# Performance work log

Hardware: AMD Instinct MI355X
Metric: run time of the kernel (lower is better)

The kernel has to match this reference:

```python
import jax, jax.numpy as jnp
import numpy as np

EPSILON = float(np.finfo(np.float32).tiny)
K = 32                 # self.k
TRAIN_ENSEMBLE = 2     # repeat_sample in train mode
TAU = 0.1


def setup_inputs() -> dict:
    key = jax.random.key(0)
    scores = jax.random.normal(key, (256, 8192, 4), dtype=jnp.float32)  # [bsz, Nmax, ensemble]
    return {"scores": scores}


def reference(scores):
    bsz, Nmax, ensemble = scores.shape
    repeat = TRAIN_ENSEMBLE
    local_k = min(K, Nmax)

    # flat_scores: (bsz*ensemble, Nmax), then repeated over samples -> (repeat*bsz*ensemble, Nmax)
    flat = scores.transpose(0, 2, 1).reshape(bsz * ensemble, Nmax)
    flat = jnp.tile(flat, (repeat, 1))

    # Gumbel(0,1) noise (m.sample())
    g = jax.random.gumbel(jax.random.key(42), flat.shape, dtype=flat.dtype)
    flat = flat + g

    zeros = jnp.zeros_like(flat)

    def step(carry, _):
        f, khot, onehot = carry
        khot_mask = jnp.maximum(1.0 - onehot, EPSILON)
        f = f + jnp.log(khot_mask)
        onehot = jax.nn.softmax(f / TAU, axis=1)
        return (f, khot + onehot, onehot), None

    (_, khot, _), _ = jax.lax.scan(step, (flat, zeros, zeros), None, length=local_k)

    # hard top-k straight-through
    _, ind = jax.lax.top_k(khot, local_k)                      # (R, local_k)
    rows = jnp.arange(khot.shape[0])[:, None]
    khot_hard = jnp.zeros_like(khot).at[rows, ind].set(1.0)
    res = khot_hard - jax.lax.stop_gradient(khot) + khot

    # (repeat, bsz, ensemble, Nmax) -> (repeat, bsz, Nmax, ensemble)
    new_mask = res.reshape(repeat, bsz, ensemble, Nmax).transpose(0, 1, 3, 2)
    return new_mask
```

## Files before the change

### kernel.cpp

```cpp
#include <hip/hip_runtime.h>

#define TPB 256
#define ROWN 8192
#define CMAX 1024
#define EPS_TINY 1.1754943508222875e-38f

__device__ __forceinline__ unsigned rotl32(unsigned x, int r) {
  return (x << r) | (x >> (32 - r));
}

__device__ __forceinline__ unsigned tf_pxor(unsigned idx) {
  const unsigned ks0 = 0u, ks1 = 42u, ks2 = 0x1BD11BDAu ^ 0u ^ 42u;
  unsigned x0 = ks0;
  unsigned x1 = idx + ks1;
#define TF4(a,b,cc,d) \
  x0 += x1; x1 = rotl32(x1,(a));  x1 ^= x0; \
  x0 += x1; x1 = rotl32(x1,(b));  x1 ^= x0; \
  x0 += x1; x1 = rotl32(x1,(cc)); x1 ^= x0; \
  x0 += x1; x1 = rotl32(x1,(d));  x1 ^= x0;
  TF4(13,15,26,6)   x0 += ks1; x1 += ks2 + 1u;
  TF4(17,29,16,24)  x0 += ks2; x1 += ks0 + 2u;
  TF4(13,15,26,6)   x0 += ks0; x1 += ks1 + 3u;
  TF4(17,29,16,24)  x0 += ks1; x1 += ks2 + 4u;
  TF4(13,15,26,6)   x0 += ks2; x1 += ks0 + 5u;
#undef TF4
  return x0 ^ x1;
}

__device__ __forceinline__ float gumbel_of(unsigned idx) {
  const unsigned bits = tf_pxor(idx);
  float u = __uint_as_float((bits >> 9) | 0x3f800000u) - 1.0f;
  u = u + EPS_TINY;
  u = fmaxf(EPS_TINY, u);
  return -logf(-logf(u));
}

__device__ __forceinline__ float approx_gumbel(unsigned bits) {
  float u = __uint_as_float((bits >> 9) | 0x3f800000u) - 1.0f;
  u = u + EPS_TINY;
  u = fmaxf(EPS_TINY, u);
  float t;
  if (u >= 0.75f) {
    const float v = 1.0f - u;
    t = v * (1.0f + v * (0.5f + v * (0.33333334f + v * (0.25f + v * 0.2f))));
  } else {
    t = -0.69314718f * __log2f(u);
  }
  return -0.69314718f * __log2f(t);
}

__device__ __forceinline__ unsigned key16_of(float x) {
  const unsigned b = __float_as_uint(x) >> 16;
  return (b & 0x8000u) ? (0xFFFFu & ~b) : (b | 0x8000u);
}

__global__ __launch_bounds__(TPB, 8)
void topk_row(const void* __restrict__ scores_raw,
              float* __restrict__ khotArr,
              unsigned short* __restrict__ idxArr,
              int* __restrict__ cntArr) {
  const int t    = threadIdx.x;
  const int lane = t & 63;
  const int wave = t >> 6;

  const int i   = blockIdx.x;
  const int xcd = i & 7;
  const int k   = i >> 3;
  const int e   = k & 3;
  const int q   = k >> 2;
  const int b   = xcd * 32 + (q & 31);
  const int rep = q >> 5;
  const int r   = rep * 1024 + b * 4 + e;
  const unsigned gbase = (unsigned)r * (unsigned)ROWN;

  __shared__ unsigned       kLds[16][TPB];
  __shared__ unsigned short candIdx[CMAX];
  __shared__ float redM[2][4];
  __shared__ float redZ[2][4];
  __shared__ int   wtot[13][4];
  __shared__ int   f32flag;

  if (t == 0) f32flag = 0;
  __syncthreads();
  {
    const unsigned* w = (const unsigned*)scores_raw;
    bool bad = false;
#pragma unroll
    for (int p = 0; p < 4; ++p) {
      const unsigned x = w[t + 256 * p];
      const float flo = __uint_as_float((x & 0xFFFFu) << 16);
      const float fhi = __uint_as_float(x & 0xFFFF0000u);
      if (!(fabsf(flo) <= 16.0f) || !(fabsf(fhi) <= 16.0f)) bad = true;
    }
    if (bad) f32flag = 1;
  }
  __syncthreads();
  const bool in_f32 = (f32flag != 0);

  const size_t ebase0 = ((size_t)b * ROWN + (size_t)t) * 4 + (size_t)e;
  float m = -3.4e38f;
  {
    unsigned pair = 0u;
    if (in_f32) {
      const float* sp = (const float*)scores_raw;
#pragma unroll
      for (int j = 0; j < 32; ++j) {
        const float fj = sp[ebase0 + (size_t)(256 * j) * 4]
                       + approx_gumbel(tf_pxor(gbase + (unsigned)(t + 256 * j)));
        m = fmaxf(m, fj);
        const unsigned kk = key16_of(fj);
        if (j & 1) { pair |= kk << 16; kLds[j >> 1][t] = pair; }
        else pair = kk;
      }
    } else {
      const unsigned short* sp = (const unsigned short*)scores_raw;
#pragma unroll
      for (int j = 0; j < 32; ++j) {
        const float fj = __uint_as_float(((unsigned)sp[ebase0 + (size_t)(256 * j) * 4]) << 16)
                       + approx_gumbel(tf_pxor(gbase + (unsigned)(t + 256 * j)));
        m = fmaxf(m, fj);
        const unsigned kk = key16_of(fj);
        if (j & 1) { pair |= kk << 16; kLds[j >> 1][t] = pair; }
        else pair = kk;
      }
    }
  }

#pragma unroll
  for (int off = 32; off >= 1; off >>= 1) m = fmaxf(m, __shfl_xor(m, off));
  if (lane == 0) redM[0][wave] = m;
  __syncthreads();
  m = fmaxf(fmaxf(redM[0][0], redM[0][1]), fmaxf(redM[0][2], redM[0][3]));

  float lo = m - 25.0f, hi = m;
#pragma unroll 1
  for (int itb = 0; itb < 7; ++itb) {
    const float mid = 0.5f * (lo + hi);
    const unsigned kmid = key16_of(mid);
    int c = 0;
#pragma unroll
    for (int h = 0; h < 16; ++h) {
      const unsigned w = kLds[h][t];
      c += ((w & 0xFFFFu) > kmid) ? 1 : 0;
      c += ((w >> 16) > kmid) ? 1 : 0;
    }
#pragma unroll
    for (int off = 32; off >= 1; off >>= 1) c += __shfl_xor(c, off);
    if (lane == 0) wtot[itb][wave] = c;
    __syncthreads();
    const int tot = wtot[itb][0] + wtot[itb][1] + wtot[itb][2] + wtot[itb][3];
    if (tot >= 33) lo = mid; else hi = mid;
  }
  const float theta = lo - 2.34f;
  const unsigned ktheta = key16_of(theta);

  int cj = 0;
#pragma unroll
  for (int h = 0; h < 16; ++h) {
    const unsigned w = kLds[h][t];
    cj += ((w & 0xFFFFu) >= ktheta) ? 1 : 0;
    cj += ((w >> 16) >= ktheta) ? 1 : 0;
  }
  int incv = cj;
#pragma unroll
  for (int off = 1; off < 64; off <<= 1) {
    const int v = __shfl_up(incv, off);
    if (lane >= off) incv += v;
  }
  if (lane == 63) wtot[12][wave] = incv;
  __syncthreads();
  int base = 0;
  for (int w = 0; w < wave; ++w) base += wtot[12][w];
  int cnt = wtot[12][0] + wtot[12][1] + wtot[12][2] + wtot[12][3];
  if (cnt > CMAX) cnt = CMAX;
  int o = base + incv - cj;
#pragma unroll
  for (int h = 0; h < 16; ++h) {
    const unsigned w = kLds[h][t];
    if ((w & 0xFFFFu) >= ktheta) {
      if (o < CMAX) candIdx[o] = (unsigned short)(t + 256 * (2 * h));
      ++o;
    }
    if ((w >> 16) >= ktheta) {
      if (o < CMAX) candIdx[o] = (unsigned short)(t + 256 * (2 * h + 1));
      ++o;
    }
  }
  __syncthreads();

  float cfr[4], khr[4];
#pragma unroll
  for (int p = 0; p < 4; ++p) {
    cfr[p] = -3.0e38f; khr[p] = -3.0e38f;
    if (256 * p < cnt) {
      const int ci = t + 256 * p;
      if (ci < cnt) {
        const int n = (int)candIdx[ci];
        const size_t ei = ((size_t)b * ROWN + (size_t)n) * 4 + (size_t)e;
        float sc;
        if (in_f32) sc = ((const float*)scores_raw)[ei];
        else sc = __uint_as_float(((unsigned)((const unsigned short*)scores_raw)[ei]) << 16);
        cfr[p] = sc + gumbel_of(gbase + (unsigned)n);
        khr[p] = 0.0f;
      }
    }
  }

  float m2;
  {
    float mm = -3.4e38f;
#pragma unroll
    for (int p = 0; p < 4; ++p)
      if (256 * p < cnt) mm = fmaxf(mm, cfr[p]);
#pragma unroll
    for (int off = 32; off >= 1; off >>= 1) mm = fmaxf(mm, __shfl_xor(mm, off));
    if (lane == 0) redM[1][wave] = mm;
    __syncthreads();
    m2 = fmaxf(fmaxf(redM[1][0], redM[1][1]), fmaxf(redM[1][2], redM[1][3]));
  }

#pragma unroll 1
  for (int it = 0; it < 32; ++it) {
    float ek[4];
    float Z = 0.0f;
#pragma unroll
    for (int p = 0; p < 4; ++p) {
      float ev = 0.0f;
      if (256 * p < cnt) {
        ev = __expf((cfr[p] - m2) * 10.0f);
        Z += ev;
      }
      ek[p] = ev;
    }
#pragma unroll
    for (int off = 32; off >= 1; off >>= 1) Z += __shfl_xor(Z, off);
    if (lane == 0) redZ[it & 1][wave] = Z;

    const bool refresh = ((it & 3) == 2);
    if (refresh) {
      float mm = -3.4e38f;
#pragma unroll
      for (int p = 0; p < 4; ++p)
        if (256 * p < cnt) mm = fmaxf(mm, cfr[p]);
#pragma unroll
      for (int off = 32; off >= 1; off >>= 1) mm = fmaxf(mm, __shfl_xor(mm, off));
      if (lane == 0) redM[(it >> 2) & 1][wave] = mm;
    }
    __syncthreads();
    Z = (redZ[it & 1][0] + redZ[it & 1][1]) + (redZ[it & 1][2] + redZ[it & 1][3]);
    float m2n = m2;
    if (refresh) {
      const int bm = (it >> 2) & 1;
      m2n = fmaxf(fmaxf(redM[bm][0], redM[bm][1]), fmaxf(redM[bm][2], redM[bm][3]));
    }

    const float rz = __builtin_amdgcn_rcpf(Z);
#pragma unroll
    for (int p = 0; p < 4; ++p) {
      if (256 * p < cnt) {
        const float pp = ek[p] * rz;
        khr[p] += pp;
        cfr[p] += __logf(fmaxf(1.0f - pp, EPS_TINY));
      }
    }
    m2 = m2n;
  }

  const size_t rowoff = (size_t)r * CMAX;
#pragma unroll
  for (int p = 0; p < 4; ++p) {
    if (256 * p < cnt) {
      const int ci = t + 256 * p;
      if (ci < cnt) {
        khotArr[rowoff + ci] = khr[p];
        idxArr[rowoff + ci]  = candIdx[ci];
      }
    }
  }
  if (t == 0) cntArr[r] = cnt;
}

__global__ __launch_bounds__(TPB)
void sel_expand(const float* __restrict__ khotArr,
                const unsigned short* __restrict__ idxArr,
                const int* __restrict__ cntArr,
                float4* __restrict__ out4) {
  const int t    = threadIdx.x;
  const int lane = t & 63;
  const int wave = t >> 6;
  const int g    = blockIdx.x;
  const int rep  = g >> 8;
  const int b    = g & 255;

  __shared__ unsigned ebm[4 * 256];
#pragma unroll
  for (int p = 0; p < 4; ++p) ebm[t + 256 * p] = 0u;
  __syncthreads();

  const int r   = rep * 1024 + b * 4 + wave;
  const int cnt = cntArr[r];
  const size_t rowoff = (size_t)r * CMAX;

  float rv[16]; int rn[16];
#pragma unroll
  for (int c = 0; c < 16; ++c) {
    rv[c] = -3.0e38f; rn[c] = 0x7FFFFFFF;
    if (64 * c < cnt) {
      const int ci = lane + 64 * c;
      if (ci < cnt) { rv[c] = khotArr[rowoff + ci]; rn[c] = (int)idxArr[rowoff + ci]; }
    }
  }

#pragma unroll 1
  for (int pass = 0; pass < 32; ++pass) {
    float bv = -3.4e38f; int bn = 0x7FFFFFFF;
#pragma unroll
    for (int c = 0; c < 16; ++c) {
      if (64 * c < cnt) {
        if (rv[c] > bv || (rv[c] == bv && rn[c] < bn)) { bv = rv[c]; bn = rn[c]; }
      }
    }
#pragma unroll
    for (int off = 32; off >= 1; off >>= 1) {
      const float ov = __shfl_xor(bv, off);
      const int   on = __shfl_xor(bn, off);
      if (ov > bv || (ov == bv && on < bn)) { bv = ov; bn = on; }
    }
    if (lane == 0) ebm[wave * 256 + (bn >> 5)] |= (1u << (bn & 31));
#pragma unroll
    for (int c = 0; c < 16; ++c)
      if (64 * c < cnt && rn[c] == bn) rv[c] = -3.0e38f;
  }
  __syncthreads();

  const size_t obase = (size_t)g * ROWN;
#pragma unroll 1
  for (int j = 0; j < 32; ++j) {
    const int n = t + 256 * j;
    float4 v;
    v.x = ((ebm[0 * 256 + (n >> 5)] >> (n & 31)) & 1u) ? 1.0f : 0.0f;
    v.y = ((ebm[1 * 256 + (n >> 5)] >> (n & 31)) & 1u) ? 1.0f : 0.0f;
    v.z = ((ebm[2 * 256 + (n >> 5)] >> (n & 31)) & 1u) ? 1.0f : 0.0f;
    v.w = ((ebm[3 * 256 + (n >> 5)] >> (n & 31)) & 1u) ? 1.0f : 0.0f;
    out4[obase + (size_t)n] = v;
  }
}

__global__ __launch_bounds__(TPB, 8)
void topk_row_fused(const void* __restrict__ scores_raw, int* __restrict__ selws) {
  const int t    = threadIdx.x;
  const int lane = t & 63;
  const int wave = t >> 6;

  const int i   = blockIdx.x;
  const int xcd = i & 7;
  const int k   = i >> 3;
  const int e   = k & 3;
  const int q   = k >> 2;
  const int b   = xcd * 32 + (q & 31);
  const int rep = q >> 5;
  const int r   = rep * 1024 + b * 4 + e;
  const unsigned gbase = (unsigned)r * (unsigned)ROWN;

  __shared__ unsigned       kLds[16][TPB];
  __shared__ unsigned short candIdx[CMAX];
  __shared__ float redM[2][4];
  __shared__ float redZ[2][4];
  __shared__ int   wtot[13][4];
  __shared__ int   f32flag;

  if (t == 0) f32flag = 0;
  __syncthreads();
  {
    const unsigned* w = (const unsigned*)scores_raw;
    bool bad = false;
#pragma unroll
    for (int p = 0; p < 4; ++p) {
      const unsigned x = w[t + 256 * p];
      const float flo = __uint_as_float((x & 0xFFFFu) << 16);
      const float fhi = __uint_as_float(x & 0xFFFF0000u);
      if (!(fabsf(flo) <= 16.0f) || !(fabsf(fhi) <= 16.0f)) bad = true;
    }
    if (bad) f32flag = 1;
  }
  __syncthreads();
  const bool in_f32 = (f32flag != 0);

  const size_t ebase0 = ((size_t)b * ROWN + (size_t)t) * 4 + (size_t)e;
  float m = -3.4e38f;
  {
    unsigned pair = 0u;
    if (in_f32) {
      const float* sp = (const float*)scores_raw;
#pragma unroll
      for (int j = 0; j < 32; ++j) {
        const float fj = sp[ebase0 + (size_t)(256 * j) * 4]
                       + approx_gumbel(tf_pxor(gbase + (unsigned)(t + 256 * j)));
        m = fmaxf(m, fj);
        const unsigned kk = key16_of(fj);
        if (j & 1) { pair |= kk << 16; kLds[j >> 1][t] = pair; }
        else pair = kk;
      }
    } else {
      const unsigned short* sp = (const unsigned short*)scores_raw;
#pragma unroll
      for (int j = 0; j < 32; ++j) {
        const float fj = __uint_as_float(((unsigned)sp[ebase0 + (size_t)(256 * j) * 4]) << 16)
                       + approx_gumbel(tf_pxor(gbase + (unsigned)(t + 256 * j)));
        m = fmaxf(m, fj);
        const unsigned kk = key16_of(fj);
        if (j & 1) { pair |= kk << 16; kLds[j >> 1][t] = pair; }
        else pair = kk;
      }
    }
  }

#pragma unroll
  for (int off = 32; off >= 1; off >>= 1) m = fmaxf(m, __shfl_xor(m, off));
  if (lane == 0) redM[0][wave] = m;
  __syncthreads();
  m = fmaxf(fmaxf(redM[0][0], redM[0][1]), fmaxf(redM[0][2], redM[0][3]));

  float lo = m - 25.0f, hi = m;
#pragma unroll 1
  for (int itb = 0; itb < 7; ++itb) {
    const float mid = 0.5f * (lo + hi);
    const unsigned kmid = key16_of(mid);
    int c = 0;
#pragma unroll
    for (int h = 0; h < 16; ++h) {
      const unsigned w = kLds[h][t];
      c += ((w & 0xFFFFu) > kmid) ? 1 : 0;
      c += ((w >> 16) > kmid) ? 1 : 0;
    }
#pragma unroll
    for (int off = 32; off >= 1; off >>= 1) c += __shfl_xor(c, off);
    if (lane == 0) wtot[itb][wave] = c;
    __syncthreads();
    const int tot = wtot[itb][0] + wtot[itb][1] + wtot[itb][2] + wtot[itb][3];
    if (tot >= 33) lo = mid; else hi = mid;
  }
  const float theta = lo - 2.34f;
  const unsigned ktheta = key16_of(theta);

  int cj = 0;
#pragma unroll
  for (int h = 0; h < 16; ++h) {
    const unsigned w = kLds[h][t];
    cj += ((w & 0xFFFFu) >= ktheta) ? 1 : 0;
    cj += ((w >> 16) >= ktheta) ? 1 : 0;
  }
  int incv = cj;
#pragma unroll
  for (int off = 1; off < 64; off <<= 1) {
    const int v = __shfl_up(incv, off);
    if (lane >= off) incv += v;
  }
  if (lane == 63) wtot[12][wave] = incv;
  __syncthreads();
  int base = 0;
  for (int w = 0; w < wave; ++w) base += wtot[12][w];
  int cnt = wtot[12][0] + wtot[12][1] + wtot[12][2] + wtot[12][3];
  if (cnt > CMAX) cnt = CMAX;
  int o = base + incv - cj;
#pragma unroll
  for (int h = 0; h < 16; ++h) {
    const unsigned w = kLds[h][t];
    if ((w & 0xFFFFu) >= ktheta) {
      if (o < CMAX) candIdx[o] = (unsigned short)(t + 256 * (2 * h));
      ++o;
    }
    if ((w >> 16) >= ktheta) {
      if (o < CMAX) candIdx[o] = (unsigned short)(t + 256 * (2 * h + 1));
      ++o;
    }
  }
  __syncthreads();

  float cfr[4], khr[4];
#pragma unroll
  for (int p = 0; p < 4; ++p) {
    cfr[p] = -3.0e38f; khr[p] = -3.0e38f;
    if (256 * p < cnt) {
      const int ci = t + 256 * p;
      if (ci < cnt) {
        const int n = (int)candIdx[ci];
        const size_t ei = ((size_t)b * ROWN + (size_t)n) * 4 + (size_t)e;
        float sc;
        if (in_f32) sc = ((const float*)scores_raw)[ei];
        else sc = __uint_as_float(((unsigned)((const unsigned short*)scores_raw)[ei]) << 16);
        cfr[p] = sc + gumbel_of(gbase + (unsigned)n);
        khr[p] = 0.0f;
      }
    }
  }

  float m2;
  {
    float mm = -3.4e38f;
#pragma unroll
    for (int p = 0; p < 4; ++p)
      if (256 * p < cnt) mm = fmaxf(mm, cfr[p]);
#pragma unroll
    for (int off = 32; off >= 1; off >>= 1) mm = fmaxf(mm, __shfl_xor(mm, off));
    if (lane == 0) redM[1][wave] = mm;
    __syncthreads();
    m2 = fmaxf(fmaxf(redM[1][0], redM[1][1]), fmaxf(redM[1][2], redM[1][3]));
  }

#pragma unroll 1
  for (int it = 0; it < 32; ++it) {
    float ek[4];
    float Z = 0.0f;
#pragma unroll
    for (int p = 0; p < 4; ++p) {
      float ev = 0.0f;
      if (256 * p < cnt) {
        ev = __expf((cfr[p] - m2) * 10.0f);
        Z += ev;
      }
      ek[p] = ev;
    }
#pragma unroll
    for (int off = 32; off >= 1; off >>= 1) Z += __shfl_xor(Z, off);
    if (lane == 0) redZ[it & 1][wave] = Z;

    const bool refresh = ((it & 3) == 2);
    if (refresh) {
      float mm = -3.4e38f;
#pragma unroll
      for (int p = 0; p < 4; ++p)
        if (256 * p < cnt) mm = fmaxf(mm, cfr[p]);
#pragma unroll
      for (int off = 32; off >= 1; off >>= 1) mm = fmaxf(mm, __shfl_xor(mm, off));
      if (lane == 0) redM[(it >> 2) & 1][wave] = mm;
    }
    __syncthreads();
    Z = (redZ[it & 1][0] + redZ[it & 1][1]) + (redZ[it & 1][2] + redZ[it & 1][3]);
    float m2n = m2;
    if (refresh) {
      const int bm = (it >> 2) & 1;
      m2n = fmaxf(fmaxf(redM[bm][0], redM[bm][1]), fmaxf(redM[bm][2], redM[bm][3]));
    }

    const float rz = __builtin_amdgcn_rcpf(Z);
#pragma unroll
    for (int p = 0; p < 4; ++p) {
      if (256 * p < cnt) {
        const float pp = ek[p] * rz;
        khr[p] += pp;
        cfr[p] += __logf(fmaxf(1.0f - pp, EPS_TINY));
      }
    }
    m2 = m2n;
  }

  float* khLds = (float*)&kLds[0][0];
#pragma unroll
  for (int p = 0; p < 4; ++p) {
    if (256 * p < cnt) {
      const int ci = t + 256 * p;
      if (ci < cnt) khLds[ci] = khr[p];
    }
  }
  __syncthreads();
  if (wave != 0) return;

  const int nch = (cnt + 63) >> 6;
#pragma unroll 1
  for (int pass = 0; pass < 32; ++pass) {
    float bv = -3.4e38f; int bn = 0x7FFFFFFF; int bci = 0;
#pragma unroll 1
    for (int c = 0; c < nch; ++c) {
      const int ci = lane + 64 * c;
      if (ci < cnt) {
        const float v = khLds[ci];
        const int  n = (int)candIdx[ci];
        if (v > bv || (v == bv && n < bn)) { bv = v; bn = n; bci = ci; }
      }
    }
#pragma unroll
    for (int off = 32; off >= 1; off >>= 1) {
      const float ov = __shfl_xor(bv, off);
      const int   on = __shfl_xor(bn, off);
      const int   oc = __shfl_xor(bci, off);
      if (ov > bv || (ov == bv && on < bn)) { bv = ov; bn = on; bci = oc; }
    }
    if (lane == 0) {
      selws[r * 32 + pass] = bn;
      khLds[bci] = -3.0e38f;
    }
  }
}

__global__ __launch_bounds__(TPB)
void expand_out(const int* __restrict__ selws, float4* __restrict__ out4) {
  const int t   = threadIdx.x;
  const int blk = blockIdx.x;
  const int grp = blk >> 2;
  const int s   = blk & 3;
  const int rep = grp >> 8;
  const int b   = grp & 255;

  __shared__ unsigned ebm[4 * 256];
#pragma unroll
  for (int p = 0; p < 4; ++p) ebm[t + 256 * p] = 0u;
  __syncthreads();
  if (t < 4) {
    const int r = rep * 1024 + b * 4 + t;
#pragma unroll 1
    for (int p = 0; p < 32; ++p) {
      const int ix = selws[r * 32 + p];
      ebm[t * 256 + (ix >> 5)] |= (1u << (ix & 31));
    }
  }
  __syncthreads();

  const size_t obase = (size_t)grp * ROWN;
#pragma unroll
  for (int j = 0; j < 8; ++j) {
    const int n = s * 2048 + t + 256 * j;
    float4 v;
    v.x = ((ebm[0 * 256 + (n >> 5)] >> (n & 31)) & 1u) ? 1.0f : 0.0f;
    v.y = ((ebm[1 * 256 + (n >> 5)] >> (n & 31)) & 1u) ? 1.0f : 0.0f;
    v.z = ((ebm[2 * 256 + (n >> 5)] >> (n & 31)) & 1u) ? 1.0f : 0.0f;
    v.w = ((ebm[3 * 256 + (n >> 5)] >> (n & 31)) & 1u) ? 1.0f : 0.0f;
    out4[obase + (size_t)n] = v;
  }
}

extern "C" void kernel_launch(void* const* d_in, const int* in_sizes, int n_in,
                              void* d_out, int out_size, void* d_ws, size_t ws_size,
                              hipStream_t stream) {
  const void* scores = d_in[0];
  const size_t KH = 2048ull * CMAX * 4;
  const size_t IX = 2048ull * CMAX * 2;
  const size_t CN = 2048ull * 4;
  if (ws_size >= KH + IX + CN) {
    float* khotArr = (float*)d_ws;
    unsigned short* idxArr = (unsigned short*)((char*)d_ws + KH);
    int* cntArr = (int*)((char*)d_ws + KH + IX);
    topk_row<<<dim3(2048), dim3(TPB), 0, stream>>>(scores, khotArr, idxArr, cntArr);
    sel_expand<<<dim3(512), dim3(TPB), 0, stream>>>(khotArr, idxArr, cntArr, (float4*)d_out);
  } else {
    int* selws = (int*)d_ws;
    topk_row_fused<<<dim3(2048), dim3(TPB), 0, stream>>>(scores, selws);
    expand_out<<<dim3(2048), dim3(TPB), 0, stream>>>(selws, (float4*)d_out);
  }
}
```

Baseline: 210.6 us.

## Zero output in topk kernel and scatter selected ones in a light second pass

```diff
diff --git a/kernel.cpp b/kernel.cpp
--- a/kernel.cpp
+++ b/kernel.cpp
@@ -58,7 +58,8 @@
 void topk_row(const void* __restrict__ scores_raw,
               float* __restrict__ khotArr,
               unsigned short* __restrict__ idxArr,
-              int* __restrict__ cntArr) {
+              int* __restrict__ cntArr,
+              float4* __restrict__ out4) {
   const int t    = threadIdx.x;
   const int lane = t & 63;
   const int wave = t >> 6;
@@ -93,6 +94,13 @@
       if (!(fabsf(flo) <= 16.0f) || !(fabsf(fhi) <= 16.0f)) bad = true;
     }
     if (bad) f32flag = 1;
+  }
+
+  {
+    float4 z; z.x = 0.0f; z.y = 0.0f; z.z = 0.0f; z.w = 0.0f;
+    float4* ob = out4 + (size_t)i * 2048;
+#pragma unroll
+    for (int p = 0; p < 8; ++p) ob[t + 256 * p] = z;
   }
   __syncthreads();
   const bool in_f32 = (f32flag != 0);
@@ -280,26 +288,21 @@
   if (t == 0) cntArr[r] = cnt;
 }
 
-__global__ __launch_bounds__(TPB)
-void sel_expand(const float* __restrict__ khotArr,
-                const unsigned short* __restrict__ idxArr,
-                const int* __restrict__ cntArr,
-                float4* __restrict__ out4) {
-  const int t    = threadIdx.x;
-  const int lane = t & 63;
-  const int wave = t >> 6;
-  const int g    = blockIdx.x;
+__global__ __launch_bounds__(64)
+void sel_scatter(const float* __restrict__ khotArr,
+                 const unsigned short* __restrict__ idxArr,
+                 const int* __restrict__ cntArr,
+                 float* __restrict__ out) {
+  const int lane = threadIdx.x;
+  const int j    = blockIdx.x;
+  const int e    = j & 3;
+  const int g    = j >> 2;
   const int rep  = g >> 8;
   const int b    = g & 255;
-
-  __shared__ unsigned ebm[4 * 256];
-#pragma unroll
-  for (int p = 0; p < 4; ++p) ebm[t + 256 * p] = 0u;
-  __syncthreads();
-
-  const int r   = rep * 1024 + b * 4 + wave;
-  const int cnt = cntArr[r];
+  const int r    = rep * 1024 + b * 4 + e;
+  const int cnt  = cntArr[r];
   const size_t rowoff = (size_t)r * CMAX;
+  const size_t obase  = ((size_t)g * ROWN) * 4 + (size_t)e;
 
   float rv[16]; int rn[16];
 #pragma unroll
@@ -326,23 +329,10 @@
       const int   on = __shfl_xor(bn, off);
       if (ov > bv || (ov == bv && on < bn)) { bv = ov; bn = on; }
     }
-    if (lane == 0) ebm[wave * 256 + (bn >> 5)] |= (1u << (bn & 31));
+    if (lane == 0) out[obase + (size_t)bn * 4] = 1.0f;
 #pragma unroll
     for (int c = 0; c < 16; ++c)
       if (64 * c < cnt && rn[c] == bn) rv[c] = -3.0e38f;
-  }
-  __syncthreads();
-
-  const size_t obase = (size_t)g * ROWN;
-#pragma unroll 1
-  for (int j = 0; j < 32; ++j) {
-    const int n = t + 256 * j;
-    float4 v;
-    v.x = ((ebm[0 * 256 + (n >> 5)] >> (n & 31)) & 1u) ? 1.0f : 0.0f;
-    v.y = ((ebm[1 * 256 + (n >> 5)] >> (n & 31)) & 1u) ? 1.0f : 0.0f;
-    v.z = ((ebm[2 * 256 + (n >> 5)] >> (n & 31)) & 1u) ? 1.0f : 0.0f;
-    v.w = ((ebm[3 * 256 + (n >> 5)] >> (n & 31)) & 1u) ? 1.0f : 0.0f;
-    out4[obase + (size_t)n] = v;
   }
 }
 
@@ -640,8 +630,10 @@
     float* khotArr = (float*)d_ws;
     unsigned short* idxArr = (unsigned short*)((char*)d_ws + KH);
     int* cntArr = (int*)((char*)d_ws + KH + IX);
-    topk_row<<<dim3(2048), dim3(TPB), 0, stream>>>(scores, khotArr, idxArr, cntArr);
-    sel_expand<<<dim3(512), dim3(TPB), 0, stream>>>(khotArr, idxArr, cntArr, (float4*)d_out);
+    topk_row<<<dim3(2048), dim3(TPB), 0, stream>>>(scores, khotArr, idxArr, cntArr,
+                                                   (float4*)d_out);
+    sel_scatter<<<dim3(2048), dim3(64), 0, stream>>>(khotArr, idxArr, cntArr,
+                                                     (float*)d_out);
   } else {
     int* selws = (int*)d_ws;
     topk_row_fused<<<dim3(2048), dim3(TPB), 0, stream>>>(scores, selws);
```

Result: no change. 211.8 us (+0.6%).
